# Kernel tuning notes

Measured on AMD Instinct MI355X. Metric: run time of the kernel, lower is better.

Reference implementation:

```python
import jax, jax.numpy as jnp
import numpy as np

WS = (4, 4, 4)          # window size (d, h, w)
NUM_HEADS = 6
DIM = 192


def _relative_position_index(ws):
    # static int index, computed in numpy
    coords = np.stack(np.meshgrid(np.arange(ws[0]), np.arange(ws[1]), np.arange(ws[2]), indexing='ij'))  # (3, wd, wh, ww)
    coords = coords.reshape(3, -1)                      # (3, N)
    rel = coords[:, :, None] - coords[:, None, :]        # (3, N, N)
    rel = rel.transpose(1, 2, 0)                         # (N, N, 3)
    rel[:, :, 0] += ws[0] - 1
    rel[:, :, 1] += ws[1] - 1
    rel[:, :, 2] += ws[2] - 1
    rel[:, :, 0] *= (2 * ws[1] - 1) * (2 * ws[2] - 1)
    rel[:, :, 1] *= (2 * ws[2] - 1)
    return rel.sum(-1)                                   # (N, N)

_REL_IDX = _relative_position_index(WS)


def setup_inputs() -> dict:
    key = jax.random.key(0)
    ks = jax.random.split(key, 4)
    x = jax.random.normal(ks[0], (2, DIM, 46, 47, 48), dtype=jnp.float32)
    qkv_w = jax.random.normal(ks[1], (3 * DIM, DIM), dtype=jnp.float32) * 0.02
    qkv_b = jnp.zeros((3 * DIM,), dtype=jnp.float32)
    proj_w = jax.random.normal(ks[2], (DIM, DIM), dtype=jnp.float32) * 0.02
    proj_b = jnp.zeros((DIM,), dtype=jnp.float32)
    rpb_table = jax.random.normal(ks[3], ((2 * WS[0] - 1) * (2 * WS[1] - 1) * (2 * WS[2] - 1), NUM_HEADS), dtype=jnp.float32) * 0.02
    return {"x": x, "qkv_w": qkv_w, "qkv_b": qkv_b, "proj_w": proj_w, "proj_b": proj_b, "rpb_table": rpb_table}


def reference(x, qkv_w, qkv_b, proj_w, proj_b, rpb_table):
    B, C, D, H, W = x.shape
    wd, wh, ww = WS
    pd = (-D) % wd
    ph = (-H) % wh
    pw = (-W) % ww
    Dp, Hp, Wp = D + pd, H + ph, W + pw

    # BCDHW -> B,D,H,W,C then pad spatial dims (zero pad, same as F.pad on BCDHW)
    xc = jnp.transpose(x, (0, 2, 3, 4, 1))
    xc = jnp.pad(xc, ((0, 0), (0, pd), (0, ph), (0, pw), (0, 0)))

    # window partition -> (nW, N, C)
    Dw, Hw, Ww = Dp // wd, Hp // wh, Wp // ww
    xw = xc.reshape(B, Dw, wd, Hw, wh, Ww, ww, C)
    xw = jnp.transpose(xw, (0, 1, 3, 5, 2, 4, 6, 7)).reshape(-1, wd * wh * ww, C)
    N = wd * wh * ww

    # windowed MHA with relative position bias
    hd = C // NUM_HEADS
    qkv = xw @ qkv_w.T + qkv_b                               # (nW, N, 3C)
    qkv = qkv.reshape(-1, N, 3, NUM_HEADS, hd)
    q, k, v = (jnp.transpose(qkv[:, :, i], (0, 2, 1, 3)) for i in range(3))  # (nW, h, N, hd)
    scale = jnp.asarray(hd, x.dtype) ** -0.5
    attn = jnp.einsum('whnd,whmd->whnm', q * scale, k)       # (nW, h, N, N)
    bias = rpb_table[_REL_IDX.reshape(-1)].reshape(N, N, NUM_HEADS)
    bias = jnp.transpose(bias, (2, 0, 1))                    # (h, N, N)
    attn = jax.nn.softmax(attn + bias[None], axis=-1)
    out = jnp.einsum('whnm,whmd->whnd', attn, v)             # (nW, h, N, hd)
    out = jnp.transpose(out, (0, 2, 1, 3)).reshape(-1, N, C)
    out = out @ proj_w.T + proj_b

    # window reverse + crop, back to BCDHW
    xr = out.reshape(B, Dw, Hw, Ww, wd, wh, ww, C)
    xr = jnp.transpose(xr, (0, 1, 4, 2, 5, 3, 6, 7)).reshape(B, Dp, Hp, Wp, C)
    xr = jnp.transpose(xr, (0, 4, 1, 2, 3))[:, :, :D, :H, :W]
    return xr
```

## Files before the change

### kernel.cpp

```cpp
#include <hip/hip_runtime.h>

typedef __bf16 bf16x8 __attribute__((ext_vector_type(8)));
typedef __bf16 bf16x4 __attribute__((ext_vector_type(4)));
typedef float  f32x4  __attribute__((ext_vector_type(4)));

#define MFMA16(a, b, c) __builtin_amdgcn_mfma_f32_16x16x32_bf16((a), (b), (c), 0, 0, 0)

constexpr int Cdim = 192, NHd = 6;
constexpr int Dd = 46, Hh = 47, Wl = 48;
constexpr int HWst = Hh * Wl;
constexpr int NWIN_PER_B = 12 * 12 * 12;
constexpr int NBLK = 2 * NWIN_PER_B;
constexpr float SCALE = 0.17677669529663687f;

constexpr int WQ_ELEMS = 576 * 192;
constexpr int WP_ELEMS = 192 * 192;
constexpr size_t OFF_WQ   = 0;
constexpr size_t OFF_WP   = OFF_WQ + WQ_ELEMS;
constexpr size_t OFF_RPBT = OFF_WP + WP_ELEMS;
constexpr size_t WS_SMALL = (OFF_RPBT + 4128) * 2;

__device__ inline bf16x8 cvt8(const float* __restrict__ p) {
  f32x4 u0 = *(const f32x4*)p;
  f32x4 u1 = *(const f32x4*)(p + 4);
  bf16x8 r;
  r[0] = (__bf16)u0[0]; r[1] = (__bf16)u0[1]; r[2] = (__bf16)u0[2]; r[3] = (__bf16)u0[3];
  r[4] = (__bf16)u1[0]; r[5] = (__bf16)u1[1]; r[6] = (__bf16)u1[2]; r[7] = (__bf16)u1[3];
  return r;
}

__device__ inline bf16x4 pack4(f32x4 v) {
  bf16x4 r;
  r[0] = (__bf16)v[0]; r[1] = (__bf16)v[1]; r[2] = (__bf16)v[2]; r[3] = (__bf16)v[3];
  return r;
}

__device__ inline bf16x8 cat8(bf16x4 a, bf16x4 b) {
  bf16x8 r;
  r[0] = a[0]; r[1] = a[1]; r[2] = a[2]; r[3] = a[3];
  r[4] = b[0]; r[5] = b[1]; r[6] = b[2]; r[7] = b[3];
  return r;
}

__global__ __launch_bounds__(256) void convert_w_kernel(
    const float* __restrict__ qkv_w, const float* __restrict__ proj_w,
    const float* __restrict__ rpb,
    __bf16* __restrict__ wq, __bf16* __restrict__ wp, float* __restrict__ rpbt) {
  const int i = blockIdx.x * 256 + threadIdx.x;
  if (i < WQ_ELEMS) wq[i] = (__bf16)qkv_w[i];
  if (i < WP_ELEMS) wp[i] = (__bf16)proj_w[i];
  if (i < 343 * NHd) {
    const int h = i / 343, idx = i % 343;
    rpbt[h * 343 + idx] = rpb[idx * NHd + h];
  }
}

constexpr int XWLD = 204;

__global__ __launch_bounds__(384, 1) void fused_kernel(
    const float* __restrict__ x, const float* __restrict__ qkv_b,
    const __bf16* __restrict__ wq, const __bf16* __restrict__ wp,
    const float* __restrict__ proj_b, const float* __restrict__ rpbt,
    float* __restrict__ out)
{
  __shared__ __bf16 xw[64 * XWLD];
  const f32x4 fz = {0.f, 0.f, 0.f, 0.f};
  const int tid = threadIdx.x, lane = tid & 63, wv = tid >> 6;
  const int li = lane & 15, g = lane >> 4;
  const int hq = wv;
  const int bid = blockIdx.x;
  const int wid = (bid & 7) * (NBLK / 8) + (bid >> 3);
  const int b = wid / NWIN_PER_B, wr = wid % NWIN_PER_B;
  const int d0 = (wr / 144) * 4, h0 = ((wr / 12) % 12) * 4, w0 = (wr % 12) * 4;

  #pragma unroll
  for (int rep = 0; rep < 8; ++rep) {
    const int task = rep * 384 + tid;
    const int c = task % Cdim, ph = task / Cdim;
    const int dd = ph >> 2, hh = ph & 3;
    const int d = d0 + dd, hs = h0 + hh;
    f32x4 v = fz;
    if (d < Dd && hs < Hh)
      v = *(const f32x4*)(x + ((size_t)(b * Cdim + c) * Dd + d) * HWst + hs * Wl + w0);
    const int nb = (dd * 16 + hh * 4) * XWLD + c;
    xw[nb]            = (__bf16)v[0];
    xw[nb + XWLD]     = (__bf16)v[1];
    xw[nb + 2 * XWLD] = (__bf16)v[2];
    xw[nb + 3 * XWLD] = (__bf16)v[3];
  }
  __syncthreads();

  bf16x8 qcat[4], kcat[4], vcat[2][2];

  {
    f32x4 acc[2][4];
    #pragma unroll
    for (int i = 0; i < 2; ++i)
      #pragma unroll
      for (int t = 0; t < 4; ++t) acc[i][t] = fz;
    #pragma unroll
    for (int kk = 0; kk < 6; ++kk) {
      const int k0 = kk * 32 + g * 8;
      bf16x8 xf[4];
      #pragma unroll
      for (int nt = 0; nt < 4; ++nt)
        xf[nt] = *(const bf16x8*)&xw[(nt * 16 + li) * XWLD + k0];
      #pragma unroll
      for (int i = 0; i < 2; ++i) {
        bf16x8 wf = *(const bf16x8*)(wq + (size_t)((hq * 2 + i) * 16 + li) * Cdim + k0);
        #pragma unroll
        for (int nt = 0; nt < 4; ++nt)
          acc[i][nt] = MFMA16(wf, xf[nt], acc[i][nt]);
      }
    }
    const f32x4 b0 = *(const f32x4*)(qkv_b + (hq * 2) * 16 + g * 4);
    const f32x4 b1 = *(const f32x4*)(qkv_b + (hq * 2 + 1) * 16 + g * 4);
    #pragma unroll
    for (int nt = 0; nt < 4; ++nt)
      qcat[nt] = cat8(pack4((acc[0][nt] + b0) * SCALE),
                      pack4((acc[1][nt] + b1) * SCALE));
  }

  {
    f32x4 acc[2][4];
    #pragma unroll
    for (int i = 0; i < 2; ++i)
      #pragma unroll
      for (int t = 0; t < 4; ++t) acc[i][t] = fz;
    #pragma unroll
    for (int kk = 0; kk < 6; ++kk) {
      const int k0 = kk * 32 + g * 8;
      bf16x8 xf[4];
      #pragma unroll
      for (int nt = 0; nt < 4; ++nt)
        xf[nt] = *(const bf16x8*)&xw[(nt * 16 + li) * XWLD + k0];
      #pragma unroll
      for (int i = 0; i < 2; ++i) {
        bf16x8 wf = *(const bf16x8*)(wq + (size_t)(192 + (hq * 2 + i) * 16 + li) * Cdim + k0);
        #pragma unroll
        for (int nt = 0; nt < 4; ++nt)
          acc[i][nt] = MFMA16(wf, xf[nt], acc[i][nt]);
      }
    }
    const f32x4 b0 = *(const f32x4*)(qkv_b + 192 + (hq * 2) * 16 + g * 4);
    const f32x4 b1 = *(const f32x4*)(qkv_b + 192 + (hq * 2 + 1) * 16 + g * 4);
    #pragma unroll
    for (int nt = 0; nt < 4; ++nt)
      kcat[nt] = cat8(pack4(acc[0][nt] + b0), pack4(acc[1][nt] + b1));
  }

  {
    f32x4 acc[2][4];
    #pragma unroll
    for (int i = 0; i < 2; ++i)
      #pragma unroll
      for (int t = 0; t < 4; ++t) acc[i][t] = fz;
    #pragma unroll
    for (int kk = 0; kk < 6; ++kk) {
      const int k0 = kk * 32 + g * 8;
      bf16x8 xf[4];
      #pragma unroll
      for (int rt = 0; rt < 4; ++rt)
        xf[rt] = *(const bf16x8*)&xw[(rt * 16 + li) * XWLD + k0];
      #pragma unroll
      for (int i = 0; i < 2; ++i) {
        bf16x8 wf = *(const bf16x8*)(wq + (size_t)(384 + (hq * 2 + i) * 16 + li) * Cdim + k0);
        #pragma unroll
        for (int rt = 0; rt < 4; ++rt)
          acc[i][rt] = MFMA16(xf[rt], wf, acc[i][rt]);
      }
    }
    const float bias0 = qkv_b[384 + (hq * 2) * 16 + li];
    const float bias1 = qkv_b[384 + (hq * 2 + 1) * 16 + li];
    const f32x4 vb0 = {bias0, bias0, bias0, bias0};
    const f32x4 vb1 = {bias1, bias1, bias1, bias1};
    #pragma unroll
    for (int i = 0; i < 2; ++i) {
      const f32x4 vb = i ? vb1 : vb0;
      vcat[i][0] = cat8(pack4(acc[i][0] + vb), pack4(acc[i][1] + vb));
      vcat[i][1] = cat8(pack4(acc[i][2] + vb), pack4(acc[i][3] + vb));
    }
  }
  __syncthreads();

  __bf16* ao = xw;

  const int hbase = ((li >> 2) - g + 3) * 7 + (li & 3) + 3;
  float brow[7][4];
  {
    const float* rp = rpbt + hq * 343 + hbase - 3;
    #pragma unroll
    for (int dd = 0; dd < 7; ++dd)
      #pragma unroll
      for (int j = 0; j < 4; ++j)
        brow[dd][j] = rp[dd * 49 + j];
  }

  #pragma unroll
  for (int rb = 0; rb < 4; ++rb) {
    f32x4 s[4];
    #pragma unroll
    for (int ct = 0; ct < 4; ++ct) s[ct] = MFMA16(kcat[ct], qcat[rb], fz);

    float t[4][4];
    float rm = -3e38f;
    #pragma unroll
    for (int ct = 0; ct < 4; ++ct) {
      #pragma unroll
      for (int r = 0; r < 4; ++r) {
        const float tv = s[ct][r] + brow[rb - ct + 3][3 - r];
        t[ct][r] = tv;
        rm = fmaxf(rm, tv);
      }
    }
    rm = fmaxf(rm, __shfl_xor(rm, 16));
    rm = fmaxf(rm, __shfl_xor(rm, 32));
    float rs = 0.f;
    #pragma unroll
    for (int ct = 0; ct < 4; ++ct)
      #pragma unroll
      for (int r = 0; r < 4; ++r) {
        const float p = __expf(t[ct][r] - rm);
        t[ct][r] = p;
        rs += p;
      }
    rs += __shfl_xor(rs, 16);
    rs += __shfl_xor(rs, 32);
    const float rinv = 1.f / rs;

    bf16x4 ppk[4];
    #pragma unroll
    for (int ct = 0; ct < 4; ++ct) {
      f32x4 pv = {t[ct][0] * rinv, t[ct][1] * rinv, t[ct][2] * rinv, t[ct][3] * rinv};
      ppk[ct] = pack4(pv);
    }
    bf16x8 pa0 = cat8(ppk[0], ppk[1]);
    bf16x8 pa1 = cat8(ppk[2], ppk[3]);

    f32x4 o0 = fz, o1 = fz;
    o0 = MFMA16(vcat[0][0], pa0, o0);
    o0 = MFMA16(vcat[0][1], pa1, o0);
    o1 = MFMA16(vcat[1][0], pa0, o1);
    o1 = MFMA16(vcat[1][1], pa1, o1);
    #pragma unroll
    for (int i = 0; i < 2; ++i) {
      const f32x4 o = i ? o1 : o0;
      *(bf16x4*)&ao[(rb * 16 + li) * XWLD + hq * 32 + i * 16 + g * 4] = pack4(o);
    }
  }
  __syncthreads();

  f32x4 pacc[2][4];
  #pragma unroll
  for (int i = 0; i < 2; ++i)
    #pragma unroll
    for (int rt = 0; rt < 4; ++rt) pacc[i][rt] = fz;
  #pragma unroll
  for (int kk = 0; kk < 6; ++kk) {
    const int k0 = kk * 32 + g * 8;
    bf16x8 af[4];
    #pragma unroll
    for (int rt = 0; rt < 4; ++rt)
      af[rt] = *(const bf16x8*)&ao[(rt * 16 + li) * XWLD + k0];
    #pragma unroll
    for (int i = 0; i < 2; ++i) {
      const int c = (wv * 2 + i) * 16 + li;
      bf16x8 bf = *(const bf16x8*)(wp + (size_t)c * Cdim + k0);
      #pragma unroll
      for (int rt = 0; rt < 4; ++rt)
        pacc[i][rt] = MFMA16(af[rt], bf, pacc[i][rt]);
    }
  }
  #pragma unroll
  for (int i = 0; i < 2; ++i) {
    const int c = (wv * 2 + i) * 16 + li;
    const float pb = proj_b[c];
    #pragma unroll
    for (int rt = 0; rt < 4; ++rt) {
      const int d = d0 + rt, hs = h0 + g;
      if (d < Dd && hs < Hh) {
        f32x4 vv = {pacc[i][rt][0] + pb, pacc[i][rt][1] + pb,
                    pacc[i][rt][2] + pb, pacc[i][rt][3] + pb};
        *(f32x4*)(out + ((size_t)(b * Cdim + c) * Dd + d) * HWst + hs * Wl + w0) = vv;
      }
    }
  }
}

constexpr int XW_LD = 200, QK_LD = 36, VT_LD = 68, P_LDF = 68;
constexpr int XW_OFF  = 0;
constexpr int Q_OFF   = 25600;
constexpr int K_OFF   = Q_OFF + 27648;
constexpr int VT_OFF  = K_OFF + 27648;
constexpr int P_OFF   = VT_OFF + 26112;
constexpr int RPB_OFF = P_OFF + 26112;
constexpr int LDS_TOTAL = RPB_OFF + 8256;

__global__ __launch_bounds__(768, 3) void winattn_fused(
    const float* __restrict__ x, const float* __restrict__ qkv_w,
    const float* __restrict__ qkv_b, const float* __restrict__ proj_w,
    const float* __restrict__ proj_b, const float* __restrict__ rpb,
    float* __restrict__ out)
{
  extern __shared__ __align__(16) char smem[];
  __bf16* xw  = (__bf16*)(smem + XW_OFF);
  __bf16* qs  = (__bf16*)(smem + Q_OFF);
  __bf16* ks  = (__bf16*)(smem + K_OFF);
  __bf16* vt  = (__bf16*)(smem + VT_OFF);
  __bf16* pl  = (__bf16*)(smem + P_OFF);
  float*  rps = (float*)(smem + RPB_OFF);
  const f32x4 fz = {0.f, 0.f, 0.f, 0.f};
  const int tid = threadIdx.x, lane = tid & 63, wv = tid >> 6;
  const int hq = wv >> 1, half = wv & 1, li = lane & 15, g = lane >> 4;
  const int bid = blockIdx.x;
  const int wid = (bid & 7) * (NBLK / 8) + (bid >> 3);
  const int b = wid / NWIN_PER_B, wr = wid % NWIN_PER_B;
  const int d0 = (wr / 144) * 4, h0 = ((wr / 12) % 12) * 4, w0 = (wr % 12) * 4;
  for (int i = tid; i < 343 * NHd; i += 768) rps[i] = rpb[i];
  #pragma unroll
  for (int rep = 0; rep < 4; ++rep) {
    const int task = rep * 768 + tid;
    const int c = task % Cdim, ph = task / Cdim;
    const int dd = ph >> 2, hh2 = ph & 3;
    const int d = d0 + dd, hsp = h0 + hh2;
    f32x4 v = fz;
    if (d < Dd && hsp < Hh)
      v = *(const f32x4*)(x + ((size_t)(b * Cdim + c) * Dd + d) * HWst + hsp * Wl + w0);
    const int nb = (dd * 16 + hh2 * 4) * XW_LD + c;
    xw[nb] = (__bf16)v[0]; xw[nb + XW_LD] = (__bf16)v[1];
    xw[nb + 2 * XW_LD] = (__bf16)v[2]; xw[nb + 3 * XW_LD] = (__bf16)v[3];
  }
  __syncthreads();
  {
    f32x4 acc[6][2];
    #pragma unroll
    for (int it = 0; it < 6; ++it)
      #pragma unroll
      for (int rr = 0; rr < 2; ++rr) acc[it][rr] = fz;
    #pragma unroll
    for (int kk = 0; kk < 6; ++kk) {
      const int k0 = kk * 32 + g * 8;
      bf16x8 af[2];
      #pragma unroll
      for (int rr = 0; rr < 2; ++rr)
        af[rr] = *(const bf16x8*)&xw[((half * 2 + rr) * 16 + li) * XW_LD + k0];
      #pragma unroll
      for (int it = 0; it < 6; ++it) {
        const int T = (it >> 1) * 12 + hq * 2 + (it & 1);
        const int j = T * 16 + li;
        bf16x8 bf = cvt8(qkv_w + j * Cdim + k0);
        #pragma unroll
        for (int rr = 0; rr < 2; ++rr) acc[it][rr] = MFMA16(af[rr], bf, acc[it][rr]);
      }
    }
    #pragma unroll
    for (int it = 0; it < 6; ++it) {
      const int part = it >> 1, e16 = (it & 1) * 16;
      const int j0 = (part * 12 + hq * 2 + (it & 1)) * 16;
      const float qb = qkv_b[j0 + li];
      #pragma unroll
      for (int rr = 0; rr < 2; ++rr) {
        const int rb = half * 2 + rr;
        #pragma unroll
        for (int r = 0; r < 4; ++r) {
          const float val = acc[it][rr][r] + qb;
          const int n = rb * 16 + g * 4 + r;
          if (part == 0)      qs[(hq * 64 + n) * QK_LD + e16 + li] = (__bf16)val;
          else if (part == 1) ks[(hq * 64 + n) * QK_LD + e16 + li] = (__bf16)val;
          else                vt[(hq * 32 + e16 + li) * VT_LD + n] = (__bf16)val;
        }
      }
    }
  }
  __syncthreads();
  {
    __bf16* pw = pl + wv * 16 * P_LDF;
    #pragma unroll 1
    for (int rr = 0; rr < 2; ++rr) {
      const int rb = half * 2 + rr;
      bf16x8 aq = *(const bf16x8*)&qs[(hq * 64 + rb * 16 + li) * QK_LD + g * 8];
      f32x4 s[4];
      #pragma unroll
      for (int ct = 0; ct < 4; ++ct) {
        bf16x8 bk = *(const bf16x8*)&ks[(hq * 64 + ct * 16 + li) * QK_LD + g * 8];
        s[ct] = MFMA16(aq, bk, fz);
      }
      float t[4][4], rm[4] = {-3e38f, -3e38f, -3e38f, -3e38f};
      #pragma unroll
      for (int ct = 0; ct < 4; ++ct) {
        #pragma unroll
        for (int r = 0; r < 4; ++r) {
          const int idx = (rb - ct + 3) * 49 + (g - (li >> 2) + 3) * 7 + (r - (li & 3) + 3);
          const float tv = s[ct][r] * SCALE + rps[idx * NHd + hq];
          t[ct][r] = tv;
          rm[r] = fmaxf(rm[r], tv);
        }
      }
      #pragma unroll
      for (int r = 0; r < 4; ++r) {
        rm[r] = fmaxf(rm[r], __shfl_xor(rm[r], 1, 16));
        rm[r] = fmaxf(rm[r], __shfl_xor(rm[r], 2, 16));
        rm[r] = fmaxf(rm[r], __shfl_xor(rm[r], 4, 16));
        rm[r] = fmaxf(rm[r], __shfl_xor(rm[r], 8, 16));
      }
      float rs[4] = {0, 0, 0, 0};
      #pragma unroll
      for (int ct = 0; ct < 4; ++ct)
        #pragma unroll
        for (int r = 0; r < 4; ++r) {
          const float p = __expf(t[ct][r] - rm[r]);
          t[ct][r] = p; rs[r] += p;
        }
      #pragma unroll
      for (int r = 0; r < 4; ++r) {
        rs[r] += __shfl_xor(rs[r], 1, 16);
        rs[r] += __shfl_xor(rs[r], 2, 16);
        rs[r] += __shfl_xor(rs[r], 4, 16);
        rs[r] += __shfl_xor(rs[r], 8, 16);
      }
      #pragma unroll
      for (int ct = 0; ct < 4; ++ct)
        #pragma unroll
        for (int r = 0; r < 4; ++r)
          pw[(g * 4 + r) * P_LDF + ct * 16 + li] = (__bf16)t[ct][r];
      f32x4 o[2] = {fz, fz};
      #pragma unroll
      for (int kk = 0; kk < 2; ++kk) {
        bf16x8 ap = *(const bf16x8*)&pw[li * P_LDF + kk * 32 + g * 8];
        #pragma unroll
        for (int ct = 0; ct < 2; ++ct) {
          bf16x8 bv = *(const bf16x8*)&vt[(hq * 32 + ct * 16 + li) * VT_LD + kk * 32 + g * 8];
          o[ct] = MFMA16(ap, bv, o[ct]);
        }
      }
      float inv[4];
      #pragma unroll
      for (int r = 0; r < 4; ++r) inv[r] = 1.f / rs[r];
      #pragma unroll
      for (int ct = 0; ct < 2; ++ct)
        #pragma unroll
        for (int r = 0; r < 4; ++r)
          xw[(rb * 16 + g * 4 + r) * XW_LD + hq * 32 + ct * 16 + li] = (__bf16)(o[ct][r] * inv[r]);
    }
  }
  __syncthreads();
  {
    f32x4 acc[4];
    #pragma unroll
    for (int rt = 0; rt < 4; ++rt) acc[rt] = fz;
    const int c = wv * 16 + li;
    #pragma unroll
    for (int kk = 0; kk < 6; ++kk) {
      const int k0 = kk * 32 + g * 8;
      bf16x8 bf = cvt8(proj_w + c * Cdim + k0);
      #pragma unroll
      for (int rt = 0; rt < 4; ++rt) {
        bf16x8 af = *(const bf16x8*)&xw[(rt * 16 + li) * XW_LD + k0];
        acc[rt] = MFMA16(af, bf, acc[rt]);
      }
    }
    const float pb = proj_b[c];
    #pragma unroll
    for (int rt = 0; rt < 4; ++rt) {
      const int d = d0 + rt, hsp = h0 + g;
      if (d < Dd && hsp < Hh) {
        f32x4 vv = {acc[rt][0] + pb, acc[rt][1] + pb, acc[rt][2] + pb, acc[rt][3] + pb};
        *(f32x4*)(out + ((size_t)(b * Cdim + c) * Dd + d) * HWst + hsp * Wl + w0) = vv;
      }
    }
  }
}

extern "C" void kernel_launch(void* const* d_in, const int* in_sizes, int n_in,
                              void* d_out, int out_size, void* d_ws, size_t ws_size,
                              hipStream_t stream) {
  const float* x      = (const float*)d_in[0];
  const float* qkv_w  = (const float*)d_in[1];
  const float* qkv_b  = (const float*)d_in[2];
  const float* proj_w = (const float*)d_in[3];
  const float* proj_b = (const float*)d_in[4];
  const float* rpb    = (const float*)d_in[5];
  float* out = (float*)d_out;

  if (ws_size >= WS_SMALL) {
    __bf16* wsb  = (__bf16*)d_ws;
    __bf16* wq   = wsb + OFF_WQ;
    __bf16* wp   = wsb + OFF_WP;
    float*  rpbt = (float*)(wsb + OFF_RPBT);
    convert_w_kernel<<<(WQ_ELEMS + 255) / 256, 256, 0, stream>>>(qkv_w, proj_w, rpb, wq, wp, rpbt);
    fused_kernel<<<NBLK, 384, 0, stream>>>(x, qkv_b, wq, wp, proj_b, rpbt, out);
  } else {
    (void)hipFuncSetAttribute(reinterpret_cast<const void*>(&winattn_fused),
                              hipFuncAttributeMaxDynamicSharedMemorySize, LDS_TOTAL);
    winattn_fused<<<NBLK, 768, LDS_TOTAL, stream>>>(
        x, qkv_w, qkv_b, proj_w, proj_b, rpb, out);
  }
}
```

Before: 322.3 us.

## Cut register pressure in fused window attention to raise occupancy

Raises the launch-bounds minimum from 1 to 5 blocks per multiprocessor, which makes the compiler cap registers per thread. To fit that cap, the QKV projections now handle one 16-row output tile at a time instead of two, and shared-memory X fragments are loaded inside the MFMA loop rather than held four at once. The relative-position bias rows are loaded one per row block instead of all seven up front, and the softmax reuses the score registers in place. The goal is more resident waves to hide memory latency, at the cost of re-reading X from LDS twice per projection and possible register spilling if the cap is too tight.

```diff
diff --git a/kernel.cpp b/kernel.cpp
--- a/kernel.cpp
+++ b/kernel.cpp
@@ -57,7 +57,7 @@
 
 constexpr int XWLD = 204;
 
-__global__ __launch_bounds__(384, 1) void fused_kernel(
+__global__ __launch_bounds__(384, 5) void fused_kernel(
     const float* __restrict__ x, const float* __restrict__ qkv_b,
     const __bf16* __restrict__ wq, const __bf16* __restrict__ wp,
     const float* __restrict__ proj_b, const float* __restrict__ rpbt,
@@ -93,124 +93,105 @@
   bf16x8 qcat[4], kcat[4], vcat[2][2];
 
   {
-    f32x4 acc[2][4];
-    #pragma unroll
-    for (int i = 0; i < 2; ++i)
-      #pragma unroll
-      for (int t = 0; t < 4; ++t) acc[i][t] = fz;
+    bf16x4 qh[2][4];
+    #pragma unroll
+    for (int i = 0; i < 2; ++i) {
+      f32x4 acc[4];
+      #pragma unroll
+      for (int t = 0; t < 4; ++t) acc[t] = fz;
+      #pragma unroll
+      for (int kk = 0; kk < 6; ++kk) {
+        const int k0 = kk * 32 + g * 8;
+        bf16x8 wf = *(const bf16x8*)(wq + (size_t)((hq * 2 + i) * 16 + li) * Cdim + k0);
+        #pragma unroll
+        for (int nt = 0; nt < 4; ++nt) {
+          bf16x8 xf = *(const bf16x8*)&xw[(nt * 16 + li) * XWLD + k0];
+          acc[nt] = MFMA16(wf, xf, acc[nt]);
+        }
+      }
+      const f32x4 bi = *(const f32x4*)(qkv_b + (hq * 2 + i) * 16 + g * 4);
+      #pragma unroll
+      for (int nt = 0; nt < 4; ++nt) qh[i][nt] = pack4((acc[nt] + bi) * SCALE);
+    }
+    #pragma unroll
+    for (int nt = 0; nt < 4; ++nt) qcat[nt] = cat8(qh[0][nt], qh[1][nt]);
+  }
+
+  {
+    bf16x4 kh[2][4];
+    #pragma unroll
+    for (int i = 0; i < 2; ++i) {
+      f32x4 acc[4];
+      #pragma unroll
+      for (int t = 0; t < 4; ++t) acc[t] = fz;
+      #pragma unroll
+      for (int kk = 0; kk < 6; ++kk) {
+        const int k0 = kk * 32 + g * 8;
+        bf16x8 wf = *(const bf16x8*)(wq + (size_t)(192 + (hq * 2 + i) * 16 + li) * Cdim + k0);
+        #pragma unroll
+        for (int nt = 0; nt < 4; ++nt) {
+          bf16x8 xf = *(const bf16x8*)&xw[(nt * 16 + li) * XWLD + k0];
+          acc[nt] = MFMA16(wf, xf, acc[nt]);
+        }
+      }
+      const f32x4 bi = *(const f32x4*)(qkv_b + 192 + (hq * 2 + i) * 16 + g * 4);
+      #pragma unroll
+      for (int nt = 0; nt < 4; ++nt) kh[i][nt] = pack4(acc[nt] + bi);
+    }
+    #pragma unroll
+    for (int nt = 0; nt < 4; ++nt) kcat[nt] = cat8(kh[0][nt], kh[1][nt]);
+  }
+
+  #pragma unroll
+  for (int i = 0; i < 2; ++i) {
+    f32x4 acc[4];
+    #pragma unroll
+    for (int t = 0; t < 4; ++t) acc[t] = fz;
     #pragma unroll
     for (int kk = 0; kk < 6; ++kk) {
       const int k0 = kk * 32 + g * 8;
-      bf16x8 xf[4];
-      #pragma unroll
-      for (int nt = 0; nt < 4; ++nt)
-        xf[nt] = *(const bf16x8*)&xw[(nt * 16 + li) * XWLD + k0];
-      #pragma unroll
-      for (int i = 0; i < 2; ++i) {
-        bf16x8 wf = *(const bf16x8*)(wq + (size_t)((hq * 2 + i) * 16 + li) * Cdim + k0);
-        #pragma unroll
-        for (int nt = 0; nt < 4; ++nt)
-          acc[i][nt] = MFMA16(wf, xf[nt], acc[i][nt]);
-      }
-    }
-    const f32x4 b0 = *(const f32x4*)(qkv_b + (hq * 2) * 16 + g * 4);
-    const f32x4 b1 = *(const f32x4*)(qkv_b + (hq * 2 + 1) * 16 + g * 4);
-    #pragma unroll
-    for (int nt = 0; nt < 4; ++nt)
-      qcat[nt] = cat8(pack4((acc[0][nt] + b0) * SCALE),
-                      pack4((acc[1][nt] + b1) * SCALE));
-  }
-
-  {
-    f32x4 acc[2][4];
-    #pragma unroll
-    for (int i = 0; i < 2; ++i)
-      #pragma unroll
-      for (int t = 0; t < 4; ++t) acc[i][t] = fz;
-    #pragma unroll
-    for (int kk = 0; kk < 6; ++kk) {
-      const int k0 = kk * 32 + g * 8;
-      bf16x8 xf[4];
-      #pragma unroll
-      for (int nt = 0; nt < 4; ++nt)
-        xf[nt] = *(const bf16x8*)&xw[(nt * 16 + li) * XWLD + k0];
-      #pragma unroll
-      for (int i = 0; i < 2; ++i) {
-        bf16x8 wf = *(const bf16x8*)(wq + (size_t)(192 + (hq * 2 + i) * 16 + li) * Cdim + k0);
-        #pragma unroll
-        for (int nt = 0; nt < 4; ++nt)
-          acc[i][nt] = MFMA16(wf, xf[nt], acc[i][nt]);
-      }
-    }
-    const f32x4 b0 = *(const f32x4*)(qkv_b + 192 + (hq * 2) * 16 + g * 4);
-    const f32x4 b1 = *(const f32x4*)(qkv_b + 192 + (hq * 2 + 1) * 16 + g * 4);
-    #pragma unroll
-    for (int nt = 0; nt < 4; ++nt)
-      kcat[nt] = cat8(pack4(acc[0][nt] + b0), pack4(acc[1][nt] + b1));
-  }
-
-  {
-    f32x4 acc[2][4];
-    #pragma unroll
-    for (int i = 0; i < 2; ++i)
-      #pragma unroll
-      for (int t = 0; t < 4; ++t) acc[i][t] = fz;
-    #pragma unroll
-    for (int kk = 0; kk < 6; ++kk) {
-      const int k0 = kk * 32 + g * 8;
-      bf16x8 xf[4];
-      #pragma unroll
-      for (int rt = 0; rt < 4; ++rt)
-        xf[rt] = *(const bf16x8*)&xw[(rt * 16 + li) * XWLD + k0];
-      #pragma unroll
-      for (int i = 0; i < 2; ++i) {
-        bf16x8 wf = *(const bf16x8*)(wq + (size_t)(384 + (hq * 2 + i) * 16 + li) * Cdim + k0);
-        #pragma unroll
-        for (int rt = 0; rt < 4; ++rt)
-          acc[i][rt] = MFMA16(xf[rt], wf, acc[i][rt]);
-      }
-    }
-    const float bias0 = qkv_b[384 + (hq * 2) * 16 + li];
-    const float bias1 = qkv_b[384 + (hq * 2 + 1) * 16 + li];
-    const f32x4 vb0 = {bias0, bias0, bias0, bias0};
-    const f32x4 vb1 = {bias1, bias1, bias1, bias1};
-    #pragma unroll
-    for (int i = 0; i < 2; ++i) {
-      const f32x4 vb = i ? vb1 : vb0;
-      vcat[i][0] = cat8(pack4(acc[i][0] + vb), pack4(acc[i][1] + vb));
-      vcat[i][1] = cat8(pack4(acc[i][2] + vb), pack4(acc[i][3] + vb));
-    }
+      bf16x8 wf = *(const bf16x8*)(wq + (size_t)(384 + (hq * 2 + i) * 16 + li) * Cdim + k0);
+      #pragma unroll
+      for (int rt = 0; rt < 4; ++rt) {
+        bf16x8 xf = *(const bf16x8*)&xw[(rt * 16 + li) * XWLD + k0];
+        acc[rt] = MFMA16(xf, wf, acc[rt]);
+      }
+    }
+    const float bias = qkv_b[384 + (hq * 2 + i) * 16 + li];
+    const f32x4 vb = {bias, bias, bias, bias};
+    vcat[i][0] = cat8(pack4(acc[0] + vb), pack4(acc[1] + vb));
+    vcat[i][1] = cat8(pack4(acc[2] + vb), pack4(acc[3] + vb));
   }
   __syncthreads();
 
   __bf16* ao = xw;
 
   const int hbase = ((li >> 2) - g + 3) * 7 + (li & 3) + 3;
+  const float* rp = rpbt + hq * 343 + hbase - 3;
   float brow[7][4];
-  {
-    const float* rp = rpbt + hq * 343 + hbase - 3;
-    #pragma unroll
-    for (int dd = 0; dd < 7; ++dd)
-      #pragma unroll
-      for (int j = 0; j < 4; ++j)
-        brow[dd][j] = rp[dd * 49 + j];
-  }
+  #pragma unroll
+  for (int dd = 0; dd < 3; ++dd)
+    #pragma unroll
+    for (int j = 0; j < 4; ++j)
+      brow[dd][j] = rp[dd * 49 + j];
 
   #pragma unroll
   for (int rb = 0; rb < 4; ++rb) {
+    #pragma unroll
+    for (int j = 0; j < 4; ++j)
+      brow[rb + 3][j] = rp[(rb + 3) * 49 + j];
+
     f32x4 s[4];
     #pragma unroll
     for (int ct = 0; ct < 4; ++ct) s[ct] = MFMA16(kcat[ct], qcat[rb], fz);
 
-    float t[4][4];
     float rm = -3e38f;
     #pragma unroll
     for (int ct = 0; ct < 4; ++ct) {
       #pragma unroll
       for (int r = 0; r < 4; ++r) {
-        const float tv = s[ct][r] + brow[rb - ct + 3][3 - r];
-        t[ct][r] = tv;
-        rm = fmaxf(rm, tv);
+        s[ct][r] += brow[rb - ct + 3][3 - r];
+        rm = fmaxf(rm, s[ct][r]);
       }
     }
     rm = fmaxf(rm, __shfl_xor(rm, 16));
@@ -220,9 +201,8 @@
     for (int ct = 0; ct < 4; ++ct)
       #pragma unroll
       for (int r = 0; r < 4; ++r) {
-        const float p = __expf(t[ct][r] - rm);
-        t[ct][r] = p;
-        rs += p;
+        s[ct][r] = __expf(s[ct][r] - rm);
+        rs += s[ct][r];
       }
     rs += __shfl_xor(rs, 16);
     rs += __shfl_xor(rs, 32);
@@ -231,7 +211,7 @@
     bf16x4 ppk[4];
     #pragma unroll
     for (int ct = 0; ct < 4; ++ct) {
-      f32x4 pv = {t[ct][0] * rinv, t[ct][1] * rinv, t[ct][2] * rinv, t[ct][3] * rinv};
+      f32x4 pv = {s[ct][0] * rinv, s[ct][1] * rinv, s[ct][2] * rinv, s[ct][3] * rinv};
       ppk[ct] = pack4(pv);
     }
     bf16x8 pa0 = cat8(ppk[0], ppk[1]);
@@ -242,11 +222,8 @@
     o0 = MFMA16(vcat[0][1], pa1, o0);
     o1 = MFMA16(vcat[1][0], pa0, o1);
     o1 = MFMA16(vcat[1][1], pa1, o1);
-    #pragma unroll
-    for (int i = 0; i < 2; ++i) {
-      const f32x4 o = i ? o1 : o0;
-      *(bf16x4*)&ao[(rb * 16 + li) * XWLD + hq * 32 + i * 16 + g * 4] = pack4(o);
-    }
+    *(bf16x4*)&ao[(rb * 16 + li) * XWLD + hq * 32 + g * 4] = pack4(o0);
+    *(bf16x4*)&ao[(rb * 16 + li) * XWLD + hq * 32 + 16 + g * 4] = pack4(o1);
   }
   __syncthreads();
 
```

Result: slower. 760.5 us (+136.0%).
